# Kernel tuning notes

Hardware: AMD Instinct MI355X
Metric: run time of the kernel (lower is better)

## Reference

```python
import jax, jax.numpy as jnp
import numpy as np

N = 100_000      # nodes
E = 1_600_000    # directed edges (avg degree 16)
F_IN = 128       # num_node_features
H = 8            # heads in conv1
C = 32           # hidden_channels
G = 64           # graphs in batch
NC = 10          # num_classes


def setup_inputs() -> dict:
    key = jax.random.key(0)
    ks = jax.random.split(key, 12)
    gl = lambda k, shape, fan: (jax.random.normal(k, shape, jnp.float32) / np.sqrt(fan)).astype(jnp.float32)
    return {
        "x": jax.random.normal(ks[0], (N, F_IN), jnp.float32),
        "edge_index": jax.random.randint(ks[1], (2, E), 0, N, dtype=jnp.int32),
        "batch": jnp.sort(jax.random.randint(ks[2], (N,), 0, G, dtype=jnp.int32)),
        "W1": gl(ks[3], (F_IN, H * C), F_IN),
        "att_src1": gl(ks[4], (H, C), C),
        "att_dst1": gl(ks[5], (H, C), C),
        "b1": jnp.zeros((H * C,), jnp.float32),
        "W2": gl(ks[6], (H * C, C), H * C),
        "att_src2": gl(ks[7], (1, C), C),
        "att_dst2": gl(ks[8], (1, C), C),
        "b2": jnp.zeros((C,), jnp.float32),
        "Wlin": gl(ks[9], (C, NC), C),
        "blin": jnp.zeros((NC,), jnp.float32),
    }


def gat_conv(x, src, dst, W, att_src, att_dst, bias, heads, ch, concat):
    """PyG GATConv (eval mode): gather, LeakyReLU(0.2) scores, segment softmax over dst, scatter-sum."""
    n = x.shape[0]
    h = (x @ W).reshape(n, heads, ch)                     # [N,H,C]
    a_s = jnp.sum(h * att_src, axis=-1)                   # [N,H]
    a_d = jnp.sum(h * att_dst, axis=-1)                   # [N,H]
    e = jax.nn.leaky_relu(a_s[src] + a_d[dst], 0.2)       # [E,H]
    m = jax.ops.segment_max(e, dst, num_segments=n)       # [N,H], stable softmax
    p = jnp.exp(e - m[dst])
    z = jax.ops.segment_sum(p, dst, num_segments=n)
    coef = p / (z[dst] + 1e-16)                           # [E,H]
    out = jax.ops.segment_sum(coef[:, :, None] * h[src], dst, num_segments=n)  # [N,H,C]
    out = out.reshape(n, heads * ch) if concat else out.mean(axis=1)
    return out + bias


def reference(x, edge_index, batch, W1, att_src1, att_dst1, b1,
              W2, att_src2, att_dst2, b2, Wlin, blin):
    n = x.shape[0]
    loops = jnp.arange(n, dtype=edge_index.dtype)         # GATConv add_self_loops=True
    src = jnp.concatenate([edge_index[0], loops])
    dst = jnp.concatenate([edge_index[1], loops])

    h = gat_conv(x, src, dst, W1, att_src1, att_dst1, b1, H, C, concat=True)
    h = jax.nn.elu(h)                                     # dropout is identity in eval
    h = gat_conv(h, src, dst, W2, att_src2, att_dst2, b2, 1, C, concat=False)

    # global_mean_pool over graph ids
    sums = jax.ops.segment_sum(h, batch, num_segments=G)  # [G,C]
    cnts = jax.ops.segment_sum(jnp.ones((n,), h.dtype), batch, num_segments=G)
    pooled = sums / jnp.maximum(cnts, 1.0)[:, None]

    return pooled @ Wlin + blin                           # [G,NC]
```

## Files before the change

kernel.cpp:

```cpp
#include <hip/hip_runtime.h>
#include <cstdint>

#define NN 100000
#define EE 1600000
#define GG 64
#define FIN 128
#define HC 256
#define NC 10
#define WS 152

typedef short v8s __attribute__((ext_vector_type(8)));
typedef float v4f __attribute__((ext_vector_type(4)));

static __device__ __forceinline__ float lrelu(float x) { return x > 0.f ? x : 0.2f * x; }
static __device__ __forceinline__ float bf2f(unsigned short b) {
  return __uint_as_float(((unsigned int)b) << 16);
}
static __device__ __forceinline__ unsigned short f2bf(float f) {
  unsigned int u = __float_as_uint(f);
  unsigned int r = (u + 0x7FFFu + ((u >> 16) & 1u)) >> 16;
  return (unsigned short)r;
}
static __device__ __forceinline__ void unpack2(unsigned int u, float& f0, float& f1) {
  f0 = __uint_as_float(u << 16);
  f1 = __uint_as_float(u & 0xFFFF0000u);
}

__global__ void k_zero(unsigned int* __restrict__ p, int n) {
  int i = blockIdx.x * 256 + threadIdx.x;
  if (i < n) p[i] = 0u;
}

__global__ __launch_bounds__(256) void k_gemm1(const float* __restrict__ x,
                                               const float* __restrict__ W1,
                                               const float* __restrict__ att_src1,
                                               const float* __restrict__ att_dst1,
                                               unsigned short* __restrict__ h1b,
                                               float* __restrict__ as1,
                                               float* __restrict__ ad1) {
  __shared__ short W1t[128 * WS];
  const int t = threadIdx.x;
  const int m0 = blockIdx.x * 64;
  const int n0 = blockIdx.y * 128;
  const int hb = blockIdx.y * 4;
  {
    const int n4 = (t & 31) * 4;
    const int kb = t >> 5;
#pragma unroll
    for (int pass = 0; pass < 16; ++pass) {
      int k = pass * 8 + kb;
      float4 v = *(const float4*)(W1 + k * HC + n0 + n4);
      W1t[(n4 + 0) * WS + k] = (short)f2bf(v.x);
      W1t[(n4 + 1) * WS + k] = (short)f2bf(v.y);
      W1t[(n4 + 2) * WS + k] = (short)f2bf(v.z);
      W1t[(n4 + 3) * WS + k] = (short)f2bf(v.w);
    }
  }
  __syncthreads();
  const int lane = t & 63;
  const int wm = t >> 6;
  const int ml = lane & 15;
  const int quad = lane >> 4;
  int row = m0 + wm * 16 + ml; if (row >= NN) row = NN - 1;
  v4f acc[8];
#pragma unroll
  for (int tt = 0; tt < 8; ++tt) acc[tt] = (v4f){0.f, 0.f, 0.f, 0.f};
#pragma unroll
  for (int kk = 0; kk < 4; ++kk) {
    const int k0 = kk * 32 + quad * 8;
    float4 lo = *(const float4*)(x + (size_t)row * FIN + k0);
    float4 hi = *(const float4*)(x + (size_t)row * FIN + k0 + 4);
    v8s a;
    a[0] = (short)f2bf(lo.x); a[1] = (short)f2bf(lo.y);
    a[2] = (short)f2bf(lo.z); a[3] = (short)f2bf(lo.w);
    a[4] = (short)f2bf(hi.x); a[5] = (short)f2bf(hi.y);
    a[6] = (short)f2bf(hi.z); a[7] = (short)f2bf(hi.w);
#pragma unroll
    for (int tt = 0; tt < 8; ++tt) {
      v8s b = *(const v8s*)&W1t[(tt * 16 + ml) * WS + k0];
      acc[tt] = __builtin_amdgcn_mfma_f32_16x16x32_bf16(a, b, acc[tt], 0, 0, 0);
    }
  }
#pragma unroll
  for (int tt = 0; tt < 8; ++tt) {
#pragma unroll
    for (int r = 0; r < 4; ++r) {
      int rg = m0 + wm * 16 + quad * 4 + r;
      if (rg < NN) h1b[(size_t)rg * HC + n0 + tt * 16 + ml] = f2bf(acc[tt][r]);
    }
  }
  float ps[4][4], pd[4][4];
#pragma unroll
  for (int i = 0; i < 4; ++i) {
#pragma unroll
    for (int r = 0; r < 4; ++r) { ps[i][r] = 0.f; pd[i][r] = 0.f; }
  }
#pragma unroll
  for (int i = 0; i < 4; ++i) {
#pragma unroll
    for (int half = 0; half < 2; ++half) {
      const int tt = 2 * i + half;
      const float a_s = att_src1[(hb + i) * 32 + half * 16 + ml];
      const float a_d = att_dst1[(hb + i) * 32 + half * 16 + ml];
#pragma unroll
      for (int r = 0; r < 4; ++r) {
        ps[i][r] += acc[tt][r] * a_s;
        pd[i][r] += acc[tt][r] * a_d;
      }
    }
  }
#pragma unroll
  for (int i = 0; i < 4; ++i) {
#pragma unroll
    for (int r = 0; r < 4; ++r) {
      float s = ps[i][r], d = pd[i][r];
      s += __shfl_xor(s, 1, 64); s += __shfl_xor(s, 2, 64);
      s += __shfl_xor(s, 4, 64); s += __shfl_xor(s, 8, 64);
      d += __shfl_xor(d, 1, 64); d += __shfl_xor(d, 2, 64);
      d += __shfl_xor(d, 4, 64); d += __shfl_xor(d, 8, 64);
      ps[i][r] = s; pd[i][r] = d;
    }
  }
  if (ml == 0) {
#pragma unroll
    for (int r = 0; r < 4; ++r) {
      int rg = m0 + wm * 16 + quad * 4 + r;
      if (rg < NN) {
#pragma unroll
        for (int i = 0; i < 4; ++i) {
          as1[rg * 8 + hb + i] = ps[i][r];
          ad1[rg * 8 + hb + i] = pd[i][r];
        }
      }
    }
  }
}

__global__ void k_count(const int* __restrict__ ei, int* __restrict__ counts) {
  int e = blockIdx.x * 256 + threadIdx.x;
  if (e < EE) atomicAdd(&counts[ei[EE + e]], 1);
}

__global__ void k_scan1(const int* __restrict__ counts, int* __restrict__ offs,
                        int* __restrict__ bsums) {
  __shared__ int s[256];
  const int t = threadIdx.x;
  const int i = blockIdx.x * 256 + t;
  int v = (i < NN) ? counts[i] : 0;
  s[t] = v;
  __syncthreads();
  for (int off = 1; off < 256; off <<= 1) {
    int tv = (t >= off) ? s[t - off] : 0;
    __syncthreads();
    s[t] += tv;
    __syncthreads();
  }
  if (i < NN) offs[i] = s[t] - v;
  if (t == 255) bsums[blockIdx.x] = s[255];
}

__global__ void k_scan2(int* __restrict__ bsums, int nb) {
  __shared__ int s[512];
  const int t = threadIdx.x;
  int v = (t < nb) ? bsums[t] : 0;
  s[t] = v;
  __syncthreads();
  for (int off = 1; off < 512; off <<= 1) {
    int tv = (t >= off) ? s[t - off] : 0;
    __syncthreads();
    s[t] += tv;
    __syncthreads();
  }
  if (t < nb) bsums[t] = s[t] - v;
}

__global__ void k_scan3(int* __restrict__ offs, const int* __restrict__ bsums,
                        int* __restrict__ cursor) {
  const int i = blockIdx.x * 256 + threadIdx.x;
  if (i < NN) {
    int v = offs[i] + bsums[i >> 8];
    offs[i] = v;
    cursor[i] = v;
  }
  if (i == 0) offs[NN] = EE;
}

__global__ void k_scatter(const int* __restrict__ ei, int* __restrict__ cursor,
                          const float* __restrict__ as1, const float* __restrict__ ad1,
                          int* __restrict__ esrc, int* __restrict__ edst,
                          float* __restrict__ wt) {
  int e = blockIdx.x * 256 + threadIdx.x;
  if (e < EE) {
    int s = ei[e];
    int d = ei[EE + e];
    int p = atomicAdd(&cursor[d], 1);
    esrc[p] = s;
    edst[p] = d;
    float4 a0 = *(const float4*)(as1 + s * 8);
    float4 a1 = *(const float4*)(as1 + s * 8 + 4);
    float4 b0 = *(const float4*)(ad1 + d * 8);
    float4 b1 = *(const float4*)(ad1 + d * 8 + 4);
    float4 r0, r1;
    r0.x = __expf(lrelu(a0.x + b0.x)); r0.y = __expf(lrelu(a0.y + b0.y));
    r0.z = __expf(lrelu(a0.z + b0.z)); r0.w = __expf(lrelu(a0.w + b0.w));
    r1.x = __expf(lrelu(a1.x + b1.x)); r1.y = __expf(lrelu(a1.y + b1.y));
    r1.z = __expf(lrelu(a1.z + b1.z)); r1.w = __expf(lrelu(a1.w + b1.w));
    *(float4*)(wt + (size_t)p * 8) = r0;
    *(float4*)(wt + (size_t)p * 8 + 4) = r1;
  }
}

__global__ __launch_bounds__(128) void k_agg1(const unsigned short* __restrict__ h1b,
                                              const float* __restrict__ as1,
                                              const float* __restrict__ ad1,
                                              const int* __restrict__ offs,
                                              const int* __restrict__ esrc,
                                              const float* __restrict__ wt,
                                              const float* __restrict__ b1,
                                              const float* __restrict__ W2,
                                              const float* __restrict__ att_src2,
                                              const float* __restrict__ att_dst2,
                                              unsigned short* __restrict__ h2b,
                                              float* __restrict__ as2,
                                              float* __restrict__ ad2) {
  __shared__ float wl[2][32][8];
  __shared__ float sv[256];
  __shared__ float zsh[2][8];
  __shared__ float sp[4][33];
  const int t = threadIdx.x;
  const int lane = t & 63;
  const int w = t >> 6;
  const int head = lane >> 3;
  const int n0 = blockIdx.x * 2;
  const int o0 = offs[n0], o1 = offs[n0 + 1], o2 = offs[n0 + 2];
  const uint2* h1u2 = (const uint2*)h1b;

  int sreg[2] = {0, 0};
  const int cnt0 = min(32, o1 - o0);
  const int cnt1 = min(32, o2 - o1);
  if (lane < cnt0) sreg[0] = esrc[o0 + lane];
  if (lane < cnt1) sreg[1] = esrc[o1 + lane];
  {
    const int j = t >> 2, hh = (t & 3) * 2;
    if (j < cnt0) *(float2*)&wl[0][j][hh] = *(const float2*)(wt + (size_t)(o0 + j) * 8 + hh);
    if (j < cnt1) *(float2*)&wl[1][j][hh] = *(const float2*)(wt + (size_t)(o1 + j) * 8 + hh);
  }
  __syncthreads();

  for (int ns = 0; ns < 2; ++ns) {
    const int n = n0 + ns;
    const int sBeg = ns ? o1 : o0;
    const int sEnd = ns ? o2 : o1;
    float acc0 = 0.f, acc1 = 0.f, acc2 = 0.f, acc3 = 0.f, z = 0.f;
    if (w == 0) {
      float w0 = __expf(lrelu(as1[n * 8 + head] + ad1[n * 8 + head]));
      z = w0;
      uint2 q = h1u2[(size_t)n * 64 + lane];
      float f0, f1, f2, f3; unpack2(q.x, f0, f1); unpack2(q.y, f2, f3);
      acc0 = w0 * f0; acc1 = w0 * f1; acc2 = w0 * f2; acc3 = w0 * f3;
    }
    int sregc = sreg[ns];
    for (int base = sBeg; base < sEnd; base += 32) {
      const int cnt = min(32, sEnd - base);
      if (base != sBeg) {
        sregc = 0;
        if (lane < cnt) sregc = esrc[base + lane];
        __syncthreads();
        const int j = t >> 2, hh = (t & 3) * 2;
        if (j < cnt) *(float2*)&wl[ns][j][hh] = *(const float2*)(wt + (size_t)(base + j) * 8 + hh);
        __syncthreads();
      }
#pragma unroll 8
      for (int j2 = w; j2 < cnt; j2 += 2) {
        int sj = __builtin_amdgcn_readlane(sregc, j2);
        uint2 q = h1u2[(size_t)sj * 64 + lane];
        float wv = wl[ns][j2][head];
        float f0, f1, f2, f3; unpack2(q.x, f0, f1); unpack2(q.y, f2, f3);
        z += wv;
        acc0 += wv * f0; acc1 += wv * f1; acc2 += wv * f2; acc3 += wv * f3;
      }
    }

    __syncthreads();
    if (w == 0) {
      *(float4*)&sv[4 * lane] = make_float4(acc0, acc1, acc2, acc3);
      if ((lane & 7) == 0) zsh[0][head] = z;
    }
    __syncthreads();
    if (w == 1) {
      float4 p = *(float4*)&sv[4 * lane];
      p.x += acc0; p.y += acc1; p.z += acc2; p.w += acc3;
      *(float4*)&sv[4 * lane] = p;
      if ((lane & 7) == 0) zsh[1][head] = z;
    }
    __syncthreads();
    {
      const int ho = t >> 4;
      const float zf = zsh[0][ho] + zsh[1][ho];
      const float zi = 1.0f / (zf + 1e-16f);
      float2 bb = *(const float2*)(b1 + 2 * t);
      float v0 = sv[2 * t] * zi + bb.x;
      float v1 = sv[2 * t + 1] * zi + bb.y;
      v0 = v0 > 0.f ? v0 : (__expf(v0) - 1.0f);
      v1 = v1 > 0.f ? v1 : (__expf(v1) - 1.0f);
      __syncthreads();
      sv[2 * t] = v0; sv[2 * t + 1] = v1;
    }
    __syncthreads();
    const int c = t & 31, rr = t >> 5;
    const float* svp = sv + rr * 64;
    const float* w2p = W2 + rr * 64 * 32 + c;
    float p = 0.f;
#pragma unroll 16
    for (int kk = 0; kk < 64; ++kk) p += svp[kk] * w2p[kk * 32];
    sp[rr][c] = p;
    __syncthreads();
    if (t < 32) {
      float hv = sp[0][t] + sp[1][t] + sp[2][t] + sp[3][t];
      h2b[(size_t)n * 32 + t] = f2bf(hv);
      float ps = hv * att_src2[t];
      float pd = hv * att_dst2[t];
#pragma unroll
      for (int m = 16; m >= 1; m >>= 1) {
        ps += __shfl_xor(ps, m, 64);
        pd += __shfl_xor(pd, m, 64);
      }
      if (t == 0) { as2[n] = ps; ad2[n] = pd; }
    }
    __syncthreads();
  }
}

__global__ void k_ew2(const int* __restrict__ esrc, const int* __restrict__ edst,
                      const float* __restrict__ as2, const float* __restrict__ ad2,
                      float* __restrict__ wt2) {
  int p = blockIdx.x * 256 + threadIdx.x;
  if (p < EE) wt2[p] = __expf(lrelu(as2[esrc[p]] + ad2[edst[p]]));
}

__global__ __launch_bounds__(256) void k_agg2(const unsigned short* __restrict__ h2b,
                                              const float* __restrict__ as2,
                                              const float* __restrict__ ad2,
                                              const int* __restrict__ offs,
                                              const int* __restrict__ esrc,
                                              const float* __restrict__ wt2,
                                              const float* __restrict__ b2,
                                              float* __restrict__ h3) {
  const int t = threadIdx.x;
  const int g = t >> 5, c = t & 31;
  const int n = blockIdx.x * 8 + g;
  const int sbase = t & 32;
  const int start = offs[n], end = offs[n + 1];
  float w0 = __expf(lrelu(as2[n] + ad2[n]));
  float z = w0;
  float acc = w0 * bf2f(h2b[(size_t)n * 32 + c]);
  for (int base = start; base < end; base += 32) {
    const int cnt = min(32, end - base);
    int s_reg = 0; float w_reg = 0.f;
    if (c < cnt) {
      s_reg = esrc[base + c];
      w_reg = wt2[base + c];
    }
#pragma unroll 8
    for (int j = 0; j < cnt; ++j) {
      int sj = __shfl(s_reg, sbase + j, 64);
      float wj = __shfl(w_reg, sbase + j, 64);
      z += wj;
      acc += wj * bf2f(h2b[(size_t)sj * 32 + c]);
    }
  }
  h3[(size_t)n * 32 + c] = acc / (z + 1e-16f) + b2[c];
}

__global__ __launch_bounds__(256) void k_poolfin(const float* __restrict__ h3,
                                                 const int* __restrict__ batch,
                                                 const float* __restrict__ Wlin,
                                                 const float* __restrict__ blin,
                                                 float* __restrict__ out) {
  __shared__ int bounds[2];
  __shared__ float red[8][33];
  __shared__ float mean[32];
  const int g = blockIdx.x;
  const int t = threadIdx.x;
  if (t < 2) {
    int target = g + t;
    int lo = 0, hi = NN;
    while (lo < hi) { int mid = (lo + hi) >> 1; if (batch[mid] < target) lo = mid + 1; else hi = mid; }
    bounds[t] = lo;
  }
  __syncthreads();
  const int lo = bounds[0], hi = bounds[1];
  const int rr = t >> 5, c = t & 31;
  float a = 0.f;
  for (int r = lo + rr; r < hi; r += 8) a += h3[(size_t)r * 32 + c];
  red[rr][c] = a;
  __syncthreads();
  if (rr == 0) {
    float s = 0.f;
#pragma unroll
    for (int i = 0; i < 8; ++i) s += red[i][c];
    float ct = (float)(hi - lo);
    ct = ct > 1.f ? ct : 1.f;
    mean[c] = s / ct;
  }
  __syncthreads();
  if (t < NC) {
    float acc = 0.f;
#pragma unroll
    for (int cc = 0; cc < 32; ++cc) acc += mean[cc] * Wlin[cc * NC + t];
    out[g * NC + t] = acc + blin[t];
  }
}

extern "C" void kernel_launch(void* const* d_in, const int* in_sizes, int n_in,
                              void* d_out, int out_size, void* d_ws, size_t ws_size,
                              hipStream_t stream) {
  const float* x        = (const float*)d_in[0];
  const int*   ei       = (const int*)d_in[1];
  const int*   batch    = (const int*)d_in[2];
  const float* W1       = (const float*)d_in[3];
  const float* att_src1 = (const float*)d_in[4];
  const float* att_dst1 = (const float*)d_in[5];
  const float* b1       = (const float*)d_in[6];
  const float* W2       = (const float*)d_in[7];
  const float* att_src2 = (const float*)d_in[8];
  const float* att_dst2 = (const float*)d_in[9];
  const float* b2       = (const float*)d_in[10];
  const float* Wlin     = (const float*)d_in[11];
  const float* blin     = (const float*)d_in[12];
  float* out = (float*)d_out;
  char* ws = (char*)d_ws;

  unsigned short* h1b = (unsigned short*)(ws + 0);
  float* as1   = (float*)(ws + 51200000);
  float* ad1   = (float*)(ws + 54400000);
  int* counts  = (int*)(ws + 57600000);
  int* offs    = (int*)(ws + 58000000);
  int* cursor  = (int*)(ws + 58400256);
  int* esrc    = (int*)(ws + 58800256);
  int* edst    = (int*)(ws + 65200256);
  int* bsums   = (int*)(ws + 71600256);
  unsigned short* h2b = (unsigned short*)(ws + 71602048);
  float* as2   = (float*)(ws + 78002048);
  float* ad2   = (float*)(ws + 78402048);
  float* wt    = (float*)(ws + 78802048);
  float* wt2   = (float*)(ws + 78802048);
  float* h3    = (float*)(ws + 85202048);

  const int nb_scan = (NN + 255) / 256;

  k_zero<<<nb_scan, 256, 0, stream>>>((unsigned int*)counts, NN);

  dim3 g1((NN + 63) / 64, 2);
  k_gemm1<<<g1, 256, 0, stream>>>(x, W1, att_src1, att_dst1, h1b, as1, ad1);

  k_count<<<(EE + 255) / 256, 256, 0, stream>>>(ei, counts);
  k_scan1<<<nb_scan, 256, 0, stream>>>(counts, offs, bsums);
  k_scan2<<<1, 512, 0, stream>>>(bsums, nb_scan);
  k_scan3<<<nb_scan, 256, 0, stream>>>(offs, bsums, cursor);
  k_scatter<<<(EE + 255) / 256, 256, 0, stream>>>(ei, cursor, as1, ad1, esrc, edst, wt);

  k_agg1<<<NN / 2, 128, 0, stream>>>(h1b, as1, ad1, offs, esrc, wt, b1, W2,
                                     att_src2, att_dst2, h2b, as2, ad2);

  k_ew2<<<(EE + 255) / 256, 256, 0, stream>>>(esrc, edst, as2, ad2, wt2);
  k_agg2<<<NN / 8, 256, 0, stream>>>(h2b, as2, ad2, offs, esrc, wt2, b2, h3);
  k_poolfin<<<GG, 256, 0, stream>>>(h3, batch, Wlin, blin, out);
}
```

Baseline: 719.0 us.

## Restructure GAT aggregation: one wave per node, fuse layer-2 edge weights, pretranspose weights

```diff
diff --git a/kernel.cpp b/kernel.cpp
--- a/kernel.cpp
+++ b/kernel.cpp
@@ -7,7 +7,6 @@
 #define FIN 128
 #define HC 256
 #define NC 10
-#define WS 152
 
 typedef short v8s __attribute__((ext_vector_type(8)));
 typedef float v4f __attribute__((ext_vector_type(4)));
@@ -31,32 +30,28 @@
   if (i < n) p[i] = 0u;
 }
 
+__global__ void k_prep(const float* __restrict__ W1, const float* __restrict__ W2,
+                       unsigned short* __restrict__ W1tg, float* __restrict__ W2t) {
+  const int b = blockIdx.x, t = threadIdx.x;
+  if (b < 256) {
+    if (t < 128) W1tg[b * 128 + t] = f2bf(W1[t * HC + b]);
+  } else {
+    const int c = b - 256;
+    W2t[c * 256 + t] = W2[t * 32 + c];
+  }
+}
+
 __global__ __launch_bounds__(256) void k_gemm1(const float* __restrict__ x,
-                                               const float* __restrict__ W1,
+                                               const unsigned short* __restrict__ W1tg,
                                                const float* __restrict__ att_src1,
                                                const float* __restrict__ att_dst1,
                                                unsigned short* __restrict__ h1b,
                                                float* __restrict__ as1,
                                                float* __restrict__ ad1) {
-  __shared__ short W1t[128 * WS];
   const int t = threadIdx.x;
   const int m0 = blockIdx.x * 64;
   const int n0 = blockIdx.y * 128;
   const int hb = blockIdx.y * 4;
-  {
-    const int n4 = (t & 31) * 4;
-    const int kb = t >> 5;
-#pragma unroll
-    for (int pass = 0; pass < 16; ++pass) {
-      int k = pass * 8 + kb;
-      float4 v = *(const float4*)(W1 + k * HC + n0 + n4);
-      W1t[(n4 + 0) * WS + k] = (short)f2bf(v.x);
-      W1t[(n4 + 1) * WS + k] = (short)f2bf(v.y);
-      W1t[(n4 + 2) * WS + k] = (short)f2bf(v.z);
-      W1t[(n4 + 3) * WS + k] = (short)f2bf(v.w);
-    }
-  }
-  __syncthreads();
   const int lane = t & 63;
   const int wm = t >> 6;
   const int ml = lane & 15;
@@ -77,7 +72,7 @@
     a[6] = (short)f2bf(hi.z); a[7] = (short)f2bf(hi.w);
 #pragma unroll
     for (int tt = 0; tt < 8; ++tt) {
-      v8s b = *(const v8s*)&W1t[(tt * 16 + ml) * WS + k0];
+      v8s b = *(const v8s*)(W1tg + (size_t)(n0 + tt * 16 + ml) * FIN + k0);
       acc[tt] = __builtin_amdgcn_mfma_f32_16x16x32_bf16(a, b, acc[tt], 0, 0, 0);
     }
   }
@@ -91,10 +86,9 @@
   }
   float ps[4][4], pd[4][4];
 #pragma unroll
-  for (int i = 0; i < 4; ++i) {
+  for (int i = 0; i < 4; ++i)
 #pragma unroll
     for (int r = 0; r < 4; ++r) { ps[i][r] = 0.f; pd[i][r] = 0.f; }
-  }
 #pragma unroll
   for (int i = 0; i < 4; ++i) {
 #pragma unroll
@@ -187,15 +181,13 @@
 
 __global__ void k_scatter(const int* __restrict__ ei, int* __restrict__ cursor,
                           const float* __restrict__ as1, const float* __restrict__ ad1,
-                          int* __restrict__ esrc, int* __restrict__ edst,
-                          float* __restrict__ wt) {
+                          int* __restrict__ esrc, float* __restrict__ wt) {
   int e = blockIdx.x * 256 + threadIdx.x;
   if (e < EE) {
     int s = ei[e];
     int d = ei[EE + e];
     int p = atomicAdd(&cursor[d], 1);
     esrc[p] = s;
-    edst[p] = d;
     float4 a0 = *(const float4*)(as1 + s * 8);
     float4 a1 = *(const float4*)(as1 + s * 8 + 4);
     float4 b0 = *(const float4*)(ad1 + d * 8);
@@ -210,132 +202,96 @@
   }
 }
 
-__global__ __launch_bounds__(128) void k_agg1(const unsigned short* __restrict__ h1b,
+__global__ __launch_bounds__(256) void k_agg1(const unsigned short* __restrict__ h1b,
                                               const float* __restrict__ as1,
                                               const float* __restrict__ ad1,
                                               const int* __restrict__ offs,
                                               const int* __restrict__ esrc,
                                               const float* __restrict__ wt,
                                               const float* __restrict__ b1,
-                                              const float* __restrict__ W2,
+                                              const float* __restrict__ W2t,
                                               const float* __restrict__ att_src2,
                                               const float* __restrict__ att_dst2,
                                               unsigned short* __restrict__ h2b,
                                               float* __restrict__ as2,
                                               float* __restrict__ ad2) {
-  __shared__ float wl[2][32][8];
-  __shared__ float sv[256];
-  __shared__ float zsh[2][8];
-  __shared__ float sp[4][33];
+  __shared__ float wl[4][64][8];
+  __shared__ float sv[4][256];
   const int t = threadIdx.x;
   const int lane = t & 63;
   const int w = t >> 6;
+  const int n = blockIdx.x * 4 + w;
   const int head = lane >> 3;
-  const int n0 = blockIdx.x * 2;
-  const int o0 = offs[n0], o1 = offs[n0 + 1], o2 = offs[n0 + 2];
+  const int start = offs[n], end = offs[n + 1];
   const uint2* h1u2 = (const uint2*)h1b;
-
-  int sreg[2] = {0, 0};
-  const int cnt0 = min(32, o1 - o0);
-  const int cnt1 = min(32, o2 - o1);
-  if (lane < cnt0) sreg[0] = esrc[o0 + lane];
-  if (lane < cnt1) sreg[1] = esrc[o1 + lane];
+  float (*wlw)[8] = wl[w];
+
+  float w0 = __expf(lrelu(as1[n * 8 + head] + ad1[n * 8 + head]));
+  float z = w0;
+  float acc0, acc1, acc2, acc3;
   {
-    const int j = t >> 2, hh = (t & 3) * 2;
-    if (j < cnt0) *(float2*)&wl[0][j][hh] = *(const float2*)(wt + (size_t)(o0 + j) * 8 + hh);
-    if (j < cnt1) *(float2*)&wl[1][j][hh] = *(const float2*)(wt + (size_t)(o1 + j) * 8 + hh);
-  }
-  __syncthreads();
-
-  for (int ns = 0; ns < 2; ++ns) {
-    const int n = n0 + ns;
-    const int sBeg = ns ? o1 : o0;
-    const int sEnd = ns ? o2 : o1;
-    float acc0 = 0.f, acc1 = 0.f, acc2 = 0.f, acc3 = 0.f, z = 0.f;
-    if (w == 0) {
-      float w0 = __expf(lrelu(as1[n * 8 + head] + ad1[n * 8 + head]));
-      z = w0;
-      uint2 q = h1u2[(size_t)n * 64 + lane];
+    uint2 q = h1u2[(size_t)n * 64 + lane];
+    float f0, f1, f2, f3; unpack2(q.x, f0, f1); unpack2(q.y, f2, f3);
+    acc0 = w0 * f0; acc1 = w0 * f1; acc2 = w0 * f2; acc3 = w0 * f3;
+  }
+
+  for (int base = start; base < end; base += 64) {
+    const int cnt = min(64, end - base);
+    int sreg = 0;
+    if (lane < cnt) {
+      sreg = esrc[base + lane];
+      float4 r0 = *(const float4*)(wt + (size_t)(base + lane) * 8);
+      float4 r1 = *(const float4*)(wt + (size_t)(base + lane) * 8 + 4);
+      *(float4*)&wlw[lane][0] = r0;
+      *(float4*)&wlw[lane][4] = r1;
+    }
+#pragma unroll 8
+    for (int j2 = 0; j2 < cnt; ++j2) {
+      int sj = __builtin_amdgcn_readlane(sreg, j2);
+      uint2 q = h1u2[(size_t)sj * 64 + lane];
+      float wv = wlw[j2][head];
       float f0, f1, f2, f3; unpack2(q.x, f0, f1); unpack2(q.y, f2, f3);
-      acc0 = w0 * f0; acc1 = w0 * f1; acc2 = w0 * f2; acc3 = w0 * f3;
-    }
-    int sregc = sreg[ns];
-    for (int base = sBeg; base < sEnd; base += 32) {
-      const int cnt = min(32, sEnd - base);
-      if (base != sBeg) {
-        sregc = 0;
-        if (lane < cnt) sregc = esrc[base + lane];
-        __syncthreads();
-        const int j = t >> 2, hh = (t & 3) * 2;
-        if (j < cnt) *(float2*)&wl[ns][j][hh] = *(const float2*)(wt + (size_t)(base + j) * 8 + hh);
-        __syncthreads();
-      }
+      z += wv;
+      acc0 += wv * f0; acc1 += wv * f1; acc2 += wv * f2; acc3 += wv * f3;
+    }
+  }
+
+  {
+    const float zi = 1.0f / (z + 1e-16f);
+    float4 bb = *(const float4*)(b1 + 4 * lane);
+    float v0 = acc0 * zi + bb.x;
+    float v1 = acc1 * zi + bb.y;
+    float v2 = acc2 * zi + bb.z;
+    float v3 = acc3 * zi + bb.w;
+    v0 = v0 > 0.f ? v0 : (__expf(v0) - 1.0f);
+    v1 = v1 > 0.f ? v1 : (__expf(v1) - 1.0f);
+    v2 = v2 > 0.f ? v2 : (__expf(v2) - 1.0f);
+    v3 = v3 > 0.f ? v3 : (__expf(v3) - 1.0f);
+    *(float4*)&sv[w][4 * lane] = make_float4(v0, v1, v2, v3);
+  }
+  {
+    const int c = lane & 31, kh = lane >> 5;
+    const float* svw = &sv[w][kh * 128];
+    const float* wtp = W2t + c * 256 + kh * 128;
+    float p = 0.f;
 #pragma unroll 8
-      for (int j2 = w; j2 < cnt; j2 += 2) {
-        int sj = __builtin_amdgcn_readlane(sregc, j2);
-        uint2 q = h1u2[(size_t)sj * 64 + lane];
-        float wv = wl[ns][j2][head];
-        float f0, f1, f2, f3; unpack2(q.x, f0, f1); unpack2(q.y, f2, f3);
-        z += wv;
-        acc0 += wv * f0; acc1 += wv * f1; acc2 += wv * f2; acc3 += wv * f3;
-      }
-    }
-
-    __syncthreads();
-    if (w == 0) {
-      *(float4*)&sv[4 * lane] = make_float4(acc0, acc1, acc2, acc3);
-      if ((lane & 7) == 0) zsh[0][head] = z;
-    }
-    __syncthreads();
-    if (w == 1) {
-      float4 p = *(float4*)&sv[4 * lane];
-      p.x += acc0; p.y += acc1; p.z += acc2; p.w += acc3;
-      *(float4*)&sv[4 * lane] = p;
-      if ((lane & 7) == 0) zsh[1][head] = z;
-    }
-    __syncthreads();
-    {
-      const int ho = t >> 4;
-      const float zf = zsh[0][ho] + zsh[1][ho];
-      const float zi = 1.0f / (zf + 1e-16f);
-      float2 bb = *(const float2*)(b1 + 2 * t);
-      float v0 = sv[2 * t] * zi + bb.x;
-      float v1 = sv[2 * t + 1] * zi + bb.y;
-      v0 = v0 > 0.f ? v0 : (__expf(v0) - 1.0f);
-      v1 = v1 > 0.f ? v1 : (__expf(v1) - 1.0f);
-      __syncthreads();
-      sv[2 * t] = v0; sv[2 * t + 1] = v1;
-    }
-    __syncthreads();
-    const int c = t & 31, rr = t >> 5;
-    const float* svp = sv + rr * 64;
-    const float* w2p = W2 + rr * 64 * 32 + c;
-    float p = 0.f;
-#pragma unroll 16
-    for (int kk = 0; kk < 64; ++kk) p += svp[kk] * w2p[kk * 32];
-    sp[rr][c] = p;
-    __syncthreads();
-    if (t < 32) {
-      float hv = sp[0][t] + sp[1][t] + sp[2][t] + sp[3][t];
-      h2b[(size_t)n * 32 + t] = f2bf(hv);
-      float ps = hv * att_src2[t];
-      float pd = hv * att_dst2[t];
-#pragma unroll
-      for (int m = 16; m >= 1; m >>= 1) {
-        ps += __shfl_xor(ps, m, 64);
-        pd += __shfl_xor(pd, m, 64);
-      }
-      if (t == 0) { as2[n] = ps; ad2[n] = pd; }
-    }
-    __syncthreads();
-  }
-}
-
-__global__ void k_ew2(const int* __restrict__ esrc, const int* __restrict__ edst,
-                      const float* __restrict__ as2, const float* __restrict__ ad2,
-                      float* __restrict__ wt2) {
-  int p = blockIdx.x * 256 + threadIdx.x;
-  if (p < EE) wt2[p] = __expf(lrelu(as2[esrc[p]] + ad2[edst[p]]));
+    for (int k4 = 0; k4 < 128; k4 += 4) {
+      float4 s4 = *(const float4*)&svw[k4];
+      float4 w4 = *(const float4*)&wtp[k4];
+      p += s4.x * w4.x + s4.y * w4.y + s4.z * w4.z + s4.w * w4.w;
+    }
+    p += __shfl_xor(p, 32, 64);
+    const float hv = p;
+    if (lane < 32) h2b[(size_t)n * 32 + lane] = f2bf(hv);
+    float ps = hv * att_src2[c];
+    float pd = hv * att_dst2[c];
+#pragma unroll
+    for (int m = 16; m >= 1; m >>= 1) {
+      ps += __shfl_xor(ps, m, 64);
+      pd += __shfl_xor(pd, m, 64);
+    }
+    if (lane == 0) { as2[n] = ps; ad2[n] = pd; }
+  }
 }
 
 __global__ __launch_bounds__(256) void k_agg2(const unsigned short* __restrict__ h2b,
@@ -343,7 +299,6 @@
                                               const float* __restrict__ ad2,
                                               const int* __restrict__ offs,
                                               const int* __restrict__ esrc,
-                                              const float* __restrict__ wt2,
                                               const float* __restrict__ b2,
                                               float* __restrict__ h3) {
   const int t = threadIdx.x;
@@ -351,7 +306,8 @@
   const int n = blockIdx.x * 8 + g;
   const int sbase = t & 32;
   const int start = offs[n], end = offs[n + 1];
-  float w0 = __expf(lrelu(as2[n] + ad2[n]));
+  const float adn = ad2[n];
+  float w0 = __expf(lrelu(as2[n] + adn));
   float z = w0;
   float acc = w0 * bf2f(h2b[(size_t)n * 32 + c]);
   for (int base = start; base < end; base += 32) {
@@ -359,7 +315,7 @@
     int s_reg = 0; float w_reg = 0.f;
     if (c < cnt) {
       s_reg = esrc[base + c];
-      w_reg = wt2[base + c];
+      w_reg = __expf(lrelu(as2[s_reg] + adn));
     }
 #pragma unroll 8
     for (int j = 0; j < cnt; ++j) {
@@ -431,39 +387,39 @@
   float* out = (float*)d_out;
   char* ws = (char*)d_ws;
 
-  unsigned short* h1b = (unsigned short*)(ws + 0);
-  float* as1   = (float*)(ws + 51200000);
-  float* ad1   = (float*)(ws + 54400000);
-  int* counts  = (int*)(ws + 57600000);
-  int* offs    = (int*)(ws + 58000000);
-  int* cursor  = (int*)(ws + 58400256);
-  int* esrc    = (int*)(ws + 58800256);
-  int* edst    = (int*)(ws + 65200256);
-  int* bsums   = (int*)(ws + 71600256);
-  unsigned short* h2b = (unsigned short*)(ws + 71602048);
-  float* as2   = (float*)(ws + 78002048);
-  float* ad2   = (float*)(ws + 78402048);
-  float* wt    = (float*)(ws + 78802048);
-  float* wt2   = (float*)(ws + 78802048);
-  float* h3    = (float*)(ws + 85202048);
+  unsigned short* h1b  = (unsigned short*)(ws + 0);
+  float* as1    = (float*)(ws + 51200000);
+  float* ad1    = (float*)(ws + 54400000);
+  int* counts   = (int*)(ws + 57600000);
+  int* offs     = (int*)(ws + 58000000);
+  int* cursor   = (int*)(ws + 58400256);
+  int* esrc     = (int*)(ws + 58800256);
+  int* bsums    = (int*)(ws + 65200256);
+  unsigned short* h2b = (unsigned short*)(ws + 65202048);
+  float* as2    = (float*)(ws + 71602048);
+  float* ad2    = (float*)(ws + 72002048);
+  unsigned short* W1tg = (unsigned short*)(ws + 72402048);
+  float* W2t    = (float*)(ws + 72467584);
+  float* wt     = (float*)(ws + 72500352);
+  float* h3     = (float*)(ws + 72500352);
 
   const int nb_scan = (NN + 255) / 256;
 
   k_zero<<<nb_scan, 256, 0, stream>>>((unsigned int*)counts, NN);
+  k_prep<<<288, 256, 0, stream>>>(W1, W2, W1tg, W2t);
 
   dim3 g1((NN + 63) / 64, 2);
-  k_gemm1<<<g1, 256, 0, stream>>>(x, W1, att_src1, att_dst1, h1b, as1, ad1);
+  k_gemm1<<<g1, 256, 0, stream>>>(x, W1tg, att_src1, att_dst1, h1b, as1, ad1);
 
   k_count<<<(EE + 255) / 256, 256, 0, stream>>>(ei, counts);
   k_scan1<<<nb_scan, 256, 0, stream>>>(counts, offs, bsums);
   k_scan2<<<1, 512, 0, stream>>>(bsums, nb_scan);
   k_scan3<<<nb_scan, 256, 0, stream>>>(offs, bsums, cursor);
-  k_scatter<<<(EE + 255) / 256, 256, 0, stream>>>(ei, cursor, as1, ad1, esrc, edst, wt);
-
-  k_agg1<<<NN / 2, 128, 0, stream>>>(h1b, as1, ad1, offs, esrc, wt, b1, W2,
+  k_scatter<<<(EE + 255) / 256, 256, 0, stream>>>(ei, cursor, as1, ad1, esrc, wt);
+
+  k_agg1<<<NN / 4, 256, 0, stream>>>(h1b, as1, ad1, offs, esrc, wt, b1, W2t,
                                      att_src2, att_dst2, h2b, as2, ad2);
 
-  k_ew2<<<(EE + 255) / 256, 256, 0, stream>>>(esrc, edst, as2, ad2, wt2);
-  k_agg2<<<NN / 8, 256, 0, stream>>>(h2b, as2, ad2, offs, esrc, wt2, b2, h3);
+  k_agg2<<<NN / 8, 256, 0, stream>>>(h2b, as2, ad2, offs, esrc, b2, h3);
   k_poolfin<<<GG, 256, 0, stream>>>(h3, batch, Wlin, blin, out);
 }
```

Measured after the change: 913.8 us. +27.1%, slower.

## Fuse layer-2 edge weights into aggregation, drop edst, pre-transpose W1 globally

Applied to the files above, without the earlier changes.

```diff
diff --git a/kernel.cpp b/kernel.cpp
--- a/kernel.cpp
+++ b/kernel.cpp
@@ -7,7 +7,6 @@
 #define FIN 128
 #define HC 256
 #define NC 10
-#define WS 152
 
 typedef short v8s __attribute__((ext_vector_type(8)));
 typedef float v4f __attribute__((ext_vector_type(4)));
@@ -31,32 +30,22 @@
   if (i < n) p[i] = 0u;
 }
 
+__global__ void k_prep(const float* __restrict__ W1, unsigned short* __restrict__ W1tg) {
+  const int b = blockIdx.x, t = threadIdx.x;
+  if (t < 128) W1tg[b * 128 + t] = f2bf(W1[t * HC + b]);
+}
+
 __global__ __launch_bounds__(256) void k_gemm1(const float* __restrict__ x,
-                                               const float* __restrict__ W1,
+                                               const unsigned short* __restrict__ W1tg,
                                                const float* __restrict__ att_src1,
                                                const float* __restrict__ att_dst1,
                                                unsigned short* __restrict__ h1b,
                                                float* __restrict__ as1,
                                                float* __restrict__ ad1) {
-  __shared__ short W1t[128 * WS];
   const int t = threadIdx.x;
   const int m0 = blockIdx.x * 64;
   const int n0 = blockIdx.y * 128;
   const int hb = blockIdx.y * 4;
-  {
-    const int n4 = (t & 31) * 4;
-    const int kb = t >> 5;
-#pragma unroll
-    for (int pass = 0; pass < 16; ++pass) {
-      int k = pass * 8 + kb;
-      float4 v = *(const float4*)(W1 + k * HC + n0 + n4);
-      W1t[(n4 + 0) * WS + k] = (short)f2bf(v.x);
-      W1t[(n4 + 1) * WS + k] = (short)f2bf(v.y);
-      W1t[(n4 + 2) * WS + k] = (short)f2bf(v.z);
-      W1t[(n4 + 3) * WS + k] = (short)f2bf(v.w);
-    }
-  }
-  __syncthreads();
   const int lane = t & 63;
   const int wm = t >> 6;
   const int ml = lane & 15;
@@ -77,7 +66,7 @@
     a[6] = (short)f2bf(hi.z); a[7] = (short)f2bf(hi.w);
 #pragma unroll
     for (int tt = 0; tt < 8; ++tt) {
-      v8s b = *(const v8s*)&W1t[(tt * 16 + ml) * WS + k0];
+      v8s b = *(const v8s*)(W1tg + (size_t)(n0 + tt * 16 + ml) * FIN + k0);
       acc[tt] = __builtin_amdgcn_mfma_f32_16x16x32_bf16(a, b, acc[tt], 0, 0, 0);
     }
   }
@@ -91,10 +80,9 @@
   }
   float ps[4][4], pd[4][4];
 #pragma unroll
-  for (int i = 0; i < 4; ++i) {
+  for (int i = 0; i < 4; ++i)
 #pragma unroll
     for (int r = 0; r < 4; ++r) { ps[i][r] = 0.f; pd[i][r] = 0.f; }
-  }
 #pragma unroll
   for (int i = 0; i < 4; ++i) {
 #pragma unroll
@@ -187,15 +175,13 @@
 
 __global__ void k_scatter(const int* __restrict__ ei, int* __restrict__ cursor,
                           const float* __restrict__ as1, const float* __restrict__ ad1,
-                          int* __restrict__ esrc, int* __restrict__ edst,
-                          float* __restrict__ wt) {
+                          int* __restrict__ esrc, float* __restrict__ wt) {
   int e = blockIdx.x * 256 + threadIdx.x;
   if (e < EE) {
     int s = ei[e];
     int d = ei[EE + e];
     int p = atomicAdd(&cursor[d], 1);
     esrc[p] = s;
-    edst[p] = d;
     float4 a0 = *(const float4*)(as1 + s * 8);
     float4 a1 = *(const float4*)(as1 + s * 8 + 4);
     float4 b0 = *(const float4*)(ad1 + d * 8);
@@ -331,19 +317,11 @@
   }
 }
 
-__global__ void k_ew2(const int* __restrict__ esrc, const int* __restrict__ edst,
-                      const float* __restrict__ as2, const float* __restrict__ ad2,
-                      float* __restrict__ wt2) {
-  int p = blockIdx.x * 256 + threadIdx.x;
-  if (p < EE) wt2[p] = __expf(lrelu(as2[esrc[p]] + ad2[edst[p]]));
-}
-
 __global__ __launch_bounds__(256) void k_agg2(const unsigned short* __restrict__ h2b,
                                               const float* __restrict__ as2,
                                               const float* __restrict__ ad2,
                                               const int* __restrict__ offs,
                                               const int* __restrict__ esrc,
-                                              const float* __restrict__ wt2,
                                               const float* __restrict__ b2,
                                               float* __restrict__ h3) {
   const int t = threadIdx.x;
@@ -351,7 +329,8 @@
   const int n = blockIdx.x * 8 + g;
   const int sbase = t & 32;
   const int start = offs[n], end = offs[n + 1];
-  float w0 = __expf(lrelu(as2[n] + ad2[n]));
+  const float adn = ad2[n];
+  float w0 = __expf(lrelu(as2[n] + adn));
   float z = w0;
   float acc = w0 * bf2f(h2b[(size_t)n * 32 + c]);
   for (int base = start; base < end; base += 32) {
@@ -359,7 +338,7 @@
     int s_reg = 0; float w_reg = 0.f;
     if (c < cnt) {
       s_reg = esrc[base + c];
-      w_reg = wt2[base + c];
+      w_reg = __expf(lrelu(as2[s_reg] + adn));
     }
 #pragma unroll 8
     for (int j = 0; j < cnt; ++j) {
@@ -431,39 +410,38 @@
   float* out = (float*)d_out;
   char* ws = (char*)d_ws;
 
-  unsigned short* h1b = (unsigned short*)(ws + 0);
-  float* as1   = (float*)(ws + 51200000);
-  float* ad1   = (float*)(ws + 54400000);
-  int* counts  = (int*)(ws + 57600000);
-  int* offs    = (int*)(ws + 58000000);
-  int* cursor  = (int*)(ws + 58400256);
-  int* esrc    = (int*)(ws + 58800256);
-  int* edst    = (int*)(ws + 65200256);
-  int* bsums   = (int*)(ws + 71600256);
-  unsigned short* h2b = (unsigned short*)(ws + 71602048);
-  float* as2   = (float*)(ws + 78002048);
-  float* ad2   = (float*)(ws + 78402048);
-  float* wt    = (float*)(ws + 78802048);
-  float* wt2   = (float*)(ws + 78802048);
-  float* h3    = (float*)(ws + 85202048);
+  unsigned short* h1b  = (unsigned short*)(ws + 0);
+  float* as1    = (float*)(ws + 51200000);
+  float* ad1    = (float*)(ws + 54400000);
+  int* counts   = (int*)(ws + 57600000);
+  int* offs     = (int*)(ws + 58000000);
+  int* cursor   = (int*)(ws + 58400256);
+  int* esrc     = (int*)(ws + 58800256);
+  int* bsums    = (int*)(ws + 65200256);
+  unsigned short* h2b = (unsigned short*)(ws + 65202048);
+  float* as2    = (float*)(ws + 71602048);
+  float* ad2    = (float*)(ws + 72002048);
+  unsigned short* W1tg = (unsigned short*)(ws + 72402048);
+  float* wt     = (float*)(ws + 72467584);
+  float* h3     = (float*)(ws + 72467584);
 
   const int nb_scan = (NN + 255) / 256;
 
   k_zero<<<nb_scan, 256, 0, stream>>>((unsigned int*)counts, NN);
+  k_prep<<<256, 128, 0, stream>>>(W1, W1tg);
 
   dim3 g1((NN + 63) / 64, 2);
-  k_gemm1<<<g1, 256, 0, stream>>>(x, W1, att_src1, att_dst1, h1b, as1, ad1);
+  k_gemm1<<<g1, 256, 0, stream>>>(x, W1tg, att_src1, att_dst1, h1b, as1, ad1);
 
   k_count<<<(EE + 255) / 256, 256, 0, stream>>>(ei, counts);
   k_scan1<<<nb_scan, 256, 0, stream>>>(counts, offs, bsums);
   k_scan2<<<1, 512, 0, stream>>>(bsums, nb_scan);
   k_scan3<<<nb_scan, 256, 0, stream>>>(offs, bsums, cursor);
-  k_scatter<<<(EE + 255) / 256, 256, 0, stream>>>(ei, cursor, as1, ad1, esrc, edst, wt);
+  k_scatter<<<(EE + 255) / 256, 256, 0, stream>>>(ei, cursor, as1, ad1, esrc, wt);
 
   k_agg1<<<NN / 2, 128, 0, stream>>>(h1b, as1, ad1, offs, esrc, wt, b1, W2,
                                      att_src2, att_dst2, h2b, as2, ad2);
 
-  k_ew2<<<(EE + 255) / 256, 256, 0, stream>>>(esrc, edst, as2, ad2, wt2);
-  k_agg2<<<NN / 8, 256, 0, stream>>>(h2b, as2, ad2, offs, esrc, wt2, b2, h3);
+  k_agg2<<<NN / 8, 256, 0, stream>>>(h2b, as2, ad2, offs, esrc, b2, h3);
   k_poolfin<<<GG, 256, 0, stream>>>(h3, batch, Wlin, blin, out);
 }
```

Measured after the change: 690.0 us. 1.04x faster.
